# Kernel optimization log

Measured on AMD Instinct MI355X. Metric: run time of the kernel, lower is better.

Reference implementation:

```python
import jax, jax.numpy as jnp
import numpy as np

LN_EPS = 1e-5


def setup_inputs() -> dict:
    key = jax.random.key(0)
    B, S, D = 4, 4096, 1024
    x = jax.random.normal(key, (B, S, D), dtype=jnp.float32)
    gamma = jnp.ones((D,), dtype=jnp.float32)
    beta = jnp.zeros((D,), dtype=jnp.float32)
    return {"x": x, "gamma": gamma, "beta": beta}


def reference(x, gamma, beta):
    # LayerNorm over last dim (embed_dim), matching nn.LayerNorm(eps=1e-5)
    mean = jnp.mean(x, axis=-1, keepdims=True)
    var = jnp.mean(jnp.square(x - mean), axis=-1, keepdims=True)
    xn = (x - mean) / jnp.sqrt(var + LN_EPS)
    xn = xn * gamma + beta
    # FFT along hidden dim then along sequence dim; keep real part.
    f = jnp.fft.fft(jnp.fft.fft(xn, axis=-1), axis=-2)
    return jnp.real(f)
```

## Files before the change

kernel.cpp:

```cpp
#include <hip/hip_runtime.h>
#include <math.h>

#define LN_EPS 1e-5f

constexpr int D = 1024;
constexpr int S = 4096;
constexpr int B = 4;
constexpr int KH = 512;
constexpr float NEG_TWO_PI = -6.283185307179586f;

__device__ __forceinline__ float2 cmul(float2 a, float2 b) {
    return make_float2(a.x * b.x - a.y * b.y, a.x * b.y + a.y * b.x);
}
__device__ __forceinline__ float2 csq(float2 a) {
    return make_float2(a.x * a.x - a.y * a.y, 2.f * a.x * a.y);
}

__device__ __forceinline__ int SWX(int a) {
    int r = a;
    r ^= (-((a >> 5) & 1)) & 5;
    r ^= (-((a >> 6) & 1)) & 10;
    r ^= (-((a >> 7) & 1)) & 17;
    return r;
}

__global__ __launch_bounds__(256) void ln_fft_d(const float* __restrict__ x,
                                                const float* __restrict__ gamma,
                                                const float* __restrict__ beta,
                                                float2* __restrict__ y) {
    __shared__ float re[D];
    __shared__ float im[D];
    __shared__ float2 twA[256];
    __shared__ float red[36];

    const int tid = threadIdx.x;
    const size_t row0 = (size_t)blockIdx.x * 2;

    {
        float sn, c;
        __sincosf(NEG_TWO_PI * (float)tid * (1.0f / 1024.0f), &sn, &c);
        twA[tid] = make_float2(c, sn);
    }

    const float4 a4 = ((const float4*)(x + row0 * D))[tid];
    const float4 c4 = ((const float4*)(x + (row0 + 1) * D))[tid];
    float s0 = a4.x + a4.y + a4.z + a4.w;
    float q0 = a4.x * a4.x + a4.y * a4.y + a4.z * a4.z + a4.w * a4.w;
    float s1 = c4.x + c4.y + c4.z + c4.w;
    float q1 = c4.x * c4.x + c4.y * c4.y + c4.z * c4.z + c4.w * c4.w;
#pragma unroll
    for (int off = 32; off; off >>= 1) {
        s0 += __shfl_down(s0, off); q0 += __shfl_down(q0, off);
        s1 += __shfl_down(s1, off); q1 += __shfl_down(q1, off);
    }
    const int wid = tid >> 6;
    if ((tid & 63) == 0) { red[wid] = s0; red[8 + wid] = q0; red[16 + wid] = s1; red[24 + wid] = q1; }
    __syncthreads();
    if (tid == 0) {
        float S0 = red[0] + red[1] + red[2] + red[3];
        float Q0 = red[8] + red[9] + red[10] + red[11];
        float S1 = red[16] + red[17] + red[18] + red[19];
        float Q1 = red[24] + red[25] + red[26] + red[27];
        float m0 = S0 * (1.0f / D), m1 = S1 * (1.0f / D);
        red[32] = m0; red[33] = rsqrtf(Q0 * (1.0f / D) - m0 * m0 + LN_EPS);
        red[34] = m1; red[35] = rsqrtf(Q1 * (1.0f / D) - m1 * m1 + LN_EPS);
    }
    __syncthreads();
    const float m0 = red[32], r0 = red[33], m1 = red[34], r1 = red[35];

    const float4 g4 = ((const float4*)gamma)[tid];
    const float4 b4 = ((const float4*)beta)[tid];
    const float av[4] = {a4.x, a4.y, a4.z, a4.w};
    const float cv[4] = {c4.x, c4.y, c4.z, c4.w};
    const float gg[4] = {g4.x, g4.y, g4.z, g4.w};
    const float bb[4] = {b4.x, b4.y, b4.z, b4.w};
#pragma unroll
    for (int j = 0; j < 4; ++j) {
        int i = 4 * tid + j;
        unsigned br = __brev((unsigned)i) >> 22;
        int dr = (int)(((br & 0x155u) << 1) | ((br & 0x2AAu) >> 1));
        int p = SWX(dr);
        re[p] = (av[j] - m0) * r0 * gg[j] + bb[j];
        im[p] = (cv[j] - m1) * r1 * gg[j] + bb[j];
    }
    __syncthreads();

#pragma unroll
    for (int st = 0; st < 5; ++st) {
        const int lq = 2 * st;
        const int q = 1 << lq;
        const int j = tid & (q - 1);
        const int i0 = ((tid & ~(q - 1)) << 2) + j;
        const int p0 = SWX(i0);
        const int p1 = SWX(i0 + q);
        const int p2 = SWX(i0 + 2 * q);
        const int p3 = SWX(i0 + 3 * q);
        const float2 w1 = twA[j << (8 - lq)];
        const float2 w2 = csq(w1);
        const float2 w3 = cmul(w1, w2);
        float2 a0 = make_float2(re[p0], im[p0]);
        float2 a1 = cmul(make_float2(re[p1], im[p1]), w1);
        float2 a2 = cmul(make_float2(re[p2], im[p2]), w2);
        float2 a3 = cmul(make_float2(re[p3], im[p3]), w3);
        float t0r = a0.x + a2.x, t0i = a0.y + a2.y;
        float t1r = a0.x - a2.x, t1i = a0.y - a2.y;
        float t2r = a1.x + a3.x, t2i = a1.y + a3.y;
        float t3r = a1.y - a3.y, t3i = a3.x - a1.x;
        re[p0] = t0r + t2r; im[p0] = t0i + t2i;
        re[p1] = t1r + t3r; im[p1] = t1i + t3i;
        re[p2] = t0r - t2r; im[p2] = t0i - t2i;
        re[p3] = t1r - t3r; im[p3] = t1i - t3i;
        __syncthreads();
    }

    float2* y0 = y + row0 * KH;
    float2* y1 = y0 + KH;
    if (tid == 0) {
        int pa = SWX(0), pb = SWX(512);
        y0[0] = make_float2(re[pa], re[pb]);
        y1[0] = make_float2(im[pa], im[pb]);
    } else {
        int kc = tid;
        int p = SWX(kc), pq = SWX(1024 - kc);
        float2 cA = make_float2(re[p], im[p]);
        float2 cB = make_float2(re[pq], im[pq]);
        y0[kc] = make_float2(0.5f * (cA.x + cB.x), 0.5f * (cA.y - cB.y));
        y1[kc] = make_float2(0.5f * (cA.y + cB.y), 0.5f * (cB.x - cA.x));
    }
    {
        int kc = tid + 256;
        int p = SWX(kc), pq = SWX(1024 - kc);
        float2 cA = make_float2(re[p], im[p]);
        float2 cB = make_float2(re[pq], im[pq]);
        y0[kc] = make_float2(0.5f * (cA.x + cB.x), 0.5f * (cA.y - cB.y));
        y1[kc] = make_float2(0.5f * (cA.y + cB.y), 0.5f * (cB.x - cA.x));
    }
}

__global__ __launch_bounds__(256) void fft_s_p1(const float2* y, float2* z) {
    __shared__ float2 tile[64 * 64];
    __shared__ float2 tw64[16];

    const int bid = blockIdx.x;
    const int dt = bid & 7;
    const int n1 = (bid >> 3) & 63;
    const int b  = bid >> 9;
    const int d0 = dt << 6;
    const int lane = threadIdx.x & 63;
    const int r4   = threadIdx.x >> 6;

    if (threadIdx.x < 16) {
        float sn, c;
        __sincosf(NEG_TWO_PI * (float)threadIdx.x * (1.0f / 64.0f), &sn, &c);
        tw64[threadIdx.x] = make_float2(c, sn);
    }

#pragma unroll
    for (int m = 0; m < 16; ++m) {
        int n2 = (m << 2) | r4;
        unsigned br = __brev((unsigned)n2) >> 26;
        int rr = (int)(((br & 0x15u) << 1) | ((br & 0x2Au) >> 1));
        tile[(rr << 6) | lane] =
            y[(size_t)((b << 12) | (n2 << 6) | n1) * KH + d0 + lane];
    }
    __syncthreads();

#pragma unroll
    for (int st = 0; st < 3; ++st) {
        const int lq = 2 * st;
        const int q = 1 << lq;
#pragma unroll
        for (int it = 0; it < 4; ++it) {
            int t = threadIdx.x + (it << 8);
            int d = t & 63;
            int bf = t >> 6;
            int j = bf & (q - 1);
            int i0 = ((bf & ~(q - 1)) << 2) + j;
            float2 w1 = tw64[j << (4 - lq)];
            float2 w2 = csq(w1);
            float2 w3 = cmul(w1, w2);
            float2 a0 = tile[(i0 << 6) | d];
            float2 a1 = cmul(tile[((i0 + q) << 6) | d], w1);
            float2 a2 = cmul(tile[((i0 + 2 * q) << 6) | d], w2);
            float2 a3 = cmul(tile[((i0 + 3 * q) << 6) | d], w3);
            float t0r = a0.x + a2.x, t0i = a0.y + a2.y;
            float t1r = a0.x - a2.x, t1i = a0.y - a2.y;
            float t2r = a1.x + a3.x, t2i = a1.y + a3.y;
            float t3r = a1.y - a3.y, t3i = a3.x - a1.x;
            tile[(i0 << 6) | d]           = make_float2(t0r + t2r, t0i + t2i);
            tile[((i0 + q) << 6) | d]     = make_float2(t1r + t3r, t1i + t3i);
            tile[((i0 + 2 * q) << 6) | d] = make_float2(t0r - t2r, t0i - t2i);
            tile[((i0 + 3 * q) << 6) | d] = make_float2(t1r - t3r, t1i - t3i);
        }
        __syncthreads();
    }

    const float ang0 = NEG_TWO_PI * (float)n1 * (1.0f / 4096.0f);
#pragma unroll
    for (int m = 0; m < 16; ++m) {
        int k2 = (m << 2) | r4;
        float2 vv = tile[(k2 << 6) | lane];
        float sn, c;
        __sincosf(ang0 * (float)k2, &sn, &c);
        z[(size_t)((b << 12) | (k2 << 6) | n1) * KH + d0 + lane] =
            make_float2(vv.x * c - vv.y * sn, vv.x * sn + vv.y * c);
    }
}

__global__ __launch_bounds__(256) void fft_s_p2(const float2* __restrict__ z,
                                                float* __restrict__ out) {
    __shared__ float2 tile[64 * 64];
    __shared__ float2 tw64[16];

    const int lane = threadIdx.x & 63;
    const int r4   = threadIdx.x >> 6;

    if (threadIdx.x < 16) {
        float sn, c;
        __sincosf(NEG_TWO_PI * (float)threadIdx.x * (1.0f / 64.0f), &sn, &c);
        tw64[threadIdx.x] = make_float2(c, sn);
    }

    if (blockIdx.x < B * 64 * 8) {
        const int bid = blockIdx.x;
        const int dt = bid & 7;
        const int k2 = (bid >> 3) & 63;
        const int b  = bid >> 9;
        const int d0 = dt << 6;

#pragma unroll
        for (int m = 0; m < 16; ++m) {
            int n1 = (m << 2) | r4;
            unsigned br = __brev((unsigned)n1) >> 26;
            int rr = (int)(((br & 0x15u) << 1) | ((br & 0x2Au) >> 1));
            tile[(rr << 6) | lane] =
                z[(size_t)((b << 12) | (k2 << 6) | n1) * KH + d0 + lane];
        }
        __syncthreads();

#pragma unroll
        for (int st = 0; st < 3; ++st) {
            const int lq = 2 * st;
            const int q = 1 << lq;
#pragma unroll
            for (int it = 0; it < 4; ++it) {
                int t = threadIdx.x + (it << 8);
                int d = t & 63;
                int bf = t >> 6;
                int j = bf & (q - 1);
                int i0 = ((bf & ~(q - 1)) << 2) + j;
                float2 w1 = tw64[j << (4 - lq)];
                float2 w2 = csq(w1);
                float2 w3 = cmul(w1, w2);
                float2 a0 = tile[(i0 << 6) | d];
                float2 a1 = cmul(tile[((i0 + q) << 6) | d], w1);
                float2 a2 = cmul(tile[((i0 + 2 * q) << 6) | d], w2);
                float2 a3 = cmul(tile[((i0 + 3 * q) << 6) | d], w3);
                float t0r = a0.x + a2.x, t0i = a0.y + a2.y;
                float t1r = a0.x - a2.x, t1i = a0.y - a2.y;
                float t2r = a1.x + a3.x, t2i = a1.y + a3.y;
                float t3r = a1.y - a3.y, t3i = a3.x - a1.x;
                tile[(i0 << 6) | d]           = make_float2(t0r + t2r, t0i + t2i);
                tile[((i0 + q) << 6) | d]     = make_float2(t1r + t3r, t1i + t3i);
                tile[((i0 + 2 * q) << 6) | d] = make_float2(t0r - t2r, t0i - t2i);
                tile[((i0 + 3 * q) << 6) | d] = make_float2(t1r - t3r, t1i - t3i);
            }
            __syncthreads();
        }

        const int kc = d0 + lane;
#pragma unroll
        for (int m = 0; m < 16; ++m) {
            int k1 = (m << 2) | r4;
            int q = (k1 << 6) | k2;
            float v = tile[(k1 << 6) | lane].x;
            if (kc) {
                out[((size_t)(b << 12) + (size_t)q) * D + kc] = v;
                int qm = (S - q) & (S - 1);
                out[((size_t)(b << 12) + (size_t)qm) * D + (D - kc)] = v;
            }
        }
    } else {
        const int b = blockIdx.x - B * 64 * 8;

#pragma unroll
        for (int m = 0; m < 16; ++m) {
            int k2 = (m << 2) | r4;
            unsigned br = __brev((unsigned)lane) >> 26;
            int rr = (int)(((br & 0x15u) << 1) | ((br & 0x2Au) >> 1));
            tile[(rr << 6) | k2] = z[(size_t)((b << 12) | (k2 << 6) | lane) * KH];
        }
        __syncthreads();

#pragma unroll
        for (int st = 0; st < 3; ++st) {
            const int lq = 2 * st;
            const int q = 1 << lq;
#pragma unroll
            for (int it = 0; it < 4; ++it) {
                int t = threadIdx.x + (it << 8);
                int d = t & 63;
                int bf = t >> 6;
                int j = bf & (q - 1);
                int i0 = ((bf & ~(q - 1)) << 2) + j;
                float2 w1 = tw64[j << (4 - lq)];
                float2 w2 = csq(w1);
                float2 w3 = cmul(w1, w2);
                float2 a0 = tile[(i0 << 6) | d];
                float2 a1 = cmul(tile[((i0 + q) << 6) | d], w1);
                float2 a2 = cmul(tile[((i0 + 2 * q) << 6) | d], w2);
                float2 a3 = cmul(tile[((i0 + 3 * q) << 6) | d], w3);
                float t0r = a0.x + a2.x, t0i = a0.y + a2.y;
                float t1r = a0.x - a2.x, t1i = a0.y - a2.y;
                float t2r = a1.x + a3.x, t2i = a1.y + a3.y;
                float t3r = a1.y - a3.y, t3i = a3.x - a1.x;
                tile[(i0 << 6) | d]           = make_float2(t0r + t2r, t0i + t2i);
                tile[((i0 + q) << 6) | d]     = make_float2(t1r + t3r, t1i + t3i);
                tile[((i0 + 2 * q) << 6) | d] = make_float2(t0r - t2r, t0i - t2i);
                tile[((i0 + 3 * q) << 6) | d] = make_float2(t1r - t3r, t1i - t3i);
            }
            __syncthreads();
        }

#pragma unroll
        for (int m = 0; m < 16; ++m) {
            int k1 = (m << 2) | r4;
            int k2 = lane;
            int q = (k1 << 6) | k2;
            int k2m = (64 - k2) & 63;
            int k1m = (k2 == 0) ? ((64 - k1) & 63) : (63 - k1);
            float2 Hq = tile[(k1 << 6) | k2];
            float2 Hm = tile[(k1m << 6) | k2m];
            size_t ob = ((size_t)(b << 12) + (size_t)q) * D;
            out[ob]       = 0.5f * (Hq.x + Hm.x);
            out[ob + 512] = 0.5f * (Hq.y + Hm.y);
        }
    }
}

extern "C" void kernel_launch(void* const* d_in, const int* in_sizes, int n_in,
                              void* d_out, int out_size, void* d_ws, size_t ws_size,
                              hipStream_t stream) {
    const float* x     = (const float*)d_in[0];
    const float* gamma = (const float*)d_in[1];
    const float* beta  = (const float*)d_in[2];
    float* out = (float*)d_out;

    float2* y = (float2*)d_ws;

    ln_fft_d<<<B * S / 2, 256, 0, stream>>>(x, gamma, beta, y);
    fft_s_p1<<<B * 64 * 8, 256, 0, stream>>>(y, y);
    fft_s_p2<<<B * 64 * 8 + B, 256, 0, stream>>>(y, out);
}
```

Before: 178.4 us.

## Restructure FFT stages: DIF radix-4 for D-axis, radix-8 two-pass for 64-point

The D-axis 1024-point FFT now uses a decimation-in-frequency radix-4 scheme on interleaved float2 shared memory with padded indexing. The first stage runs from registers, and the output is read back in digit-reversed order. The 64-point S-axis FFTs move from three radix-4 stages to two radix-8 passes with a twiddle table of 64 entries, which cuts shared-memory round trips and barriers. The inter-pass twiddle in fft_s_p1 is now built by recurrence multiplication instead of one sincos per element, which adds a small accumulated rounding error.

```diff
diff --git a/kernel.cpp b/kernel.cpp
--- a/kernel.cpp
+++ b/kernel.cpp
@@ -8,6 +8,7 @@
 constexpr int B = 4;
 constexpr int KH = 512;
 constexpr float NEG_TWO_PI = -6.283185307179586f;
+constexpr float RSQ2 = 0.70710678118654752f;
 
 __device__ __forceinline__ float2 cmul(float2 a, float2 b) {
     return make_float2(a.x * b.x - a.y * b.y, a.x * b.y + a.y * b.x);
@@ -15,39 +16,101 @@
 __device__ __forceinline__ float2 csq(float2 a) {
     return make_float2(a.x * a.x - a.y * a.y, 2.f * a.x * a.y);
 }
-
-__device__ __forceinline__ int SWX(int a) {
-    int r = a;
-    r ^= (-((a >> 5) & 1)) & 5;
-    r ^= (-((a >> 6) & 1)) & 10;
-    r ^= (-((a >> 7) & 1)) & 17;
-    return r;
+__device__ __forceinline__ float2 cadd(float2 a, float2 b) { return make_float2(a.x + b.x, a.y + b.y); }
+__device__ __forceinline__ float2 csub(float2 a, float2 b) { return make_float2(a.x - b.x, a.y - b.y); }
+__device__ __forceinline__ float2 cnegi(float2 a) { return make_float2(a.y, -a.x); }
+__device__ __forceinline__ float2 cposi(float2 a) { return make_float2(-a.y, a.x); }
+
+__device__ __forceinline__ int P(int a) { return a + (a >> 4); }
+
+__device__ __forceinline__ int rev4_10(int v) {
+    unsigned br = __brev((unsigned)v) >> 22;
+    return (int)(((br & 0x155u) << 1) | ((br & 0x2AAu) >> 1));
+}
+
+__device__ __forceinline__ void dft8(float2& c0, float2& c1, float2& c2, float2& c3,
+                                     float2& c4, float2& c5, float2& c6, float2& c7) {
+    float2 t0 = cadd(c0, c4), t1 = csub(c0, c4);
+    float2 t2 = cadd(c2, c6), t3 = csub(c2, c6);
+    float2 t4 = cadd(c1, c5), t5 = csub(c1, c5);
+    float2 t6 = cadd(c3, c7), t7 = csub(c3, c7);
+    float2 E0 = cadd(t0, t2), E2 = csub(t0, t2);
+    float2 E1 = cadd(t1, cnegi(t3)), E3 = cadd(t1, cposi(t3));
+    float2 O0 = cadd(t4, t6), O2 = csub(t4, t6);
+    float2 O1 = cadd(t5, cnegi(t7)), O3 = cadd(t5, cposi(t7));
+    float2 W1O1 = make_float2(RSQ2 * (O1.x + O1.y), RSQ2 * (O1.y - O1.x));
+    float2 W2O2 = cnegi(O2);
+    float2 W3O3 = make_float2(RSQ2 * (O3.y - O3.x), -RSQ2 * (O3.x + O3.y));
+    c0 = cadd(E0, O0); c4 = csub(E0, O0);
+    c1 = cadd(E1, W1O1); c5 = csub(E1, W1O1);
+    c2 = cadd(E2, W2O2); c6 = csub(E2, W2O2);
+    c3 = cadd(E3, W3O3); c7 = csub(E3, W3O3);
+}
+
+__device__ __forceinline__ void fft64_rows(float2* tile, const float2* tw64) {
+#pragma unroll
+    for (int h = 0; h < 2; ++h) {
+        int bf = threadIdx.x + (h << 8);
+        int col = bf & 63;
+        int g = bf >> 6;
+#define R0(mm) tile[((((g) << 3) | (mm)) << 6) | col]
+        float2 c0 = R0(0), c1 = R0(1), c2 = R0(2), c3 = R0(3);
+        float2 c4 = R0(4), c5 = R0(5), c6 = R0(6), c7 = R0(7);
+        dft8(c0, c1, c2, c3, c4, c5, c6, c7);
+        R0(0) = c0; R0(1) = c1; R0(2) = c2; R0(3) = c3;
+        R0(4) = c4; R0(5) = c5; R0(6) = c6; R0(7) = c7;
+#undef R0
+    }
+    __syncthreads();
+#pragma unroll
+    for (int h = 0; h < 2; ++h) {
+        int bf = threadIdx.x + (h << 8);
+        int col = bf & 63;
+        int j = bf >> 6;
+#define R1(mm) tile[(((j) + ((mm) << 3)) << 6) | col]
+        float2 c0 = R1(0);
+        float2 c1 = cmul(R1(1), tw64[j]);
+        float2 c2 = cmul(R1(2), tw64[2 * j]);
+        float2 c3 = cmul(R1(3), tw64[3 * j]);
+        float2 c4 = cmul(R1(4), tw64[4 * j]);
+        float2 c5 = cmul(R1(5), tw64[5 * j]);
+        float2 c6 = cmul(R1(6), tw64[6 * j]);
+        float2 c7 = cmul(R1(7), tw64[7 * j]);
+        dft8(c0, c1, c2, c3, c4, c5, c6, c7);
+        R1(0) = c0; R1(1) = c1; R1(2) = c2; R1(3) = c3;
+        R1(4) = c4; R1(5) = c5; R1(6) = c6; R1(7) = c7;
+#undef R1
+    }
+    __syncthreads();
 }
 
 __global__ __launch_bounds__(256) void ln_fft_d(const float* __restrict__ x,
                                                 const float* __restrict__ gamma,
                                                 const float* __restrict__ beta,
                                                 float2* __restrict__ y) {
-    __shared__ float re[D];
-    __shared__ float im[D];
+    __shared__ float2 cx[1088];
     __shared__ float2 twA[256];
     __shared__ float red[36];
 
     const int tid = threadIdx.x;
     const size_t row0 = (size_t)blockIdx.x * 2;
-
-    {
-        float sn, c;
-        __sincosf(NEG_TWO_PI * (float)tid * (1.0f / 1024.0f), &sn, &c);
-        twA[tid] = make_float2(c, sn);
-    }
-
-    const float4 a4 = ((const float4*)(x + row0 * D))[tid];
-    const float4 c4 = ((const float4*)(x + (row0 + 1) * D))[tid];
-    float s0 = a4.x + a4.y + a4.z + a4.w;
-    float q0 = a4.x * a4.x + a4.y * a4.y + a4.z * a4.z + a4.w * a4.w;
-    float s1 = c4.x + c4.y + c4.z + c4.w;
-    float q1 = c4.x * c4.x + c4.y * c4.y + c4.z * c4.z + c4.w * c4.w;
+    const float* x0 = x + row0 * D;
+    const float* x1 = x0 + D;
+
+    float wsn, wcs;
+    __sincosf(NEG_TWO_PI * (float)tid * (1.0f / 1024.0f), &wsn, &wcs);
+    const float2 w1s0 = make_float2(wcs, wsn);
+    twA[tid] = w1s0;
+
+    float a0[4], a1[4];
+    float s0 = 0.f, q0 = 0.f, s1 = 0.f, q1 = 0.f;
+#pragma unroll
+    for (int j = 0; j < 4; ++j) {
+        float u = x0[tid + (j << 8)];
+        float v = x1[tid + (j << 8)];
+        a0[j] = u; a1[j] = v;
+        s0 += u; q0 += u * u; s1 += v; q1 += v * v;
+    }
 #pragma unroll
     for (int off = 32; off; off >>= 1) {
         s0 += __shfl_down(s0, off); q0 += __shfl_down(q0, off);
@@ -68,78 +131,86 @@
     __syncthreads();
     const float m0 = red[32], r0 = red[33], m1 = red[34], r1 = red[35];
 
-    const float4 g4 = ((const float4*)gamma)[tid];
-    const float4 b4 = ((const float4*)beta)[tid];
-    const float av[4] = {a4.x, a4.y, a4.z, a4.w};
-    const float cv[4] = {c4.x, c4.y, c4.z, c4.w};
-    const float gg[4] = {g4.x, g4.y, g4.z, g4.w};
-    const float bb[4] = {b4.x, b4.y, b4.z, b4.w};
-#pragma unroll
-    for (int j = 0; j < 4; ++j) {
-        int i = 4 * tid + j;
-        unsigned br = __brev((unsigned)i) >> 22;
-        int dr = (int)(((br & 0x155u) << 1) | ((br & 0x2AAu) >> 1));
-        int p = SWX(dr);
-        re[p] = (av[j] - m0) * r0 * gg[j] + bb[j];
-        im[p] = (cv[j] - m1) * r1 * gg[j] + bb[j];
-    }
-    __syncthreads();
-
-#pragma unroll
-    for (int st = 0; st < 5; ++st) {
-        const int lq = 2 * st;
-        const int q = 1 << lq;
-        const int j = tid & (q - 1);
-        const int i0 = ((tid & ~(q - 1)) << 2) + j;
-        const int p0 = SWX(i0);
-        const int p1 = SWX(i0 + q);
-        const int p2 = SWX(i0 + 2 * q);
-        const int p3 = SWX(i0 + 3 * q);
-        const float2 w1 = twA[j << (8 - lq)];
-        const float2 w2 = csq(w1);
-        const float2 w3 = cmul(w1, w2);
-        float2 a0 = make_float2(re[p0], im[p0]);
-        float2 a1 = cmul(make_float2(re[p1], im[p1]), w1);
-        float2 a2 = cmul(make_float2(re[p2], im[p2]), w2);
-        float2 a3 = cmul(make_float2(re[p3], im[p3]), w3);
-        float t0r = a0.x + a2.x, t0i = a0.y + a2.y;
-        float t1r = a0.x - a2.x, t1i = a0.y - a2.y;
-        float t2r = a1.x + a3.x, t2i = a1.y + a3.y;
-        float t3r = a1.y - a3.y, t3i = a3.x - a1.x;
-        re[p0] = t0r + t2r; im[p0] = t0i + t2i;
-        re[p1] = t1r + t3r; im[p1] = t1i + t3i;
-        re[p2] = t0r - t2r; im[p2] = t0i - t2i;
-        re[p3] = t1r - t3r; im[p3] = t1i - t3i;
+    float2 A0, A1, A2, A3;
+    {
+        float gg, bb;
+        gg = gamma[tid];       bb = beta[tid];
+        A0 = make_float2((a0[0] - m0) * r0 * gg + bb, (a1[0] - m1) * r1 * gg + bb);
+        gg = gamma[tid + 256]; bb = beta[tid + 256];
+        A1 = make_float2((a0[1] - m0) * r0 * gg + bb, (a1[1] - m1) * r1 * gg + bb);
+        gg = gamma[tid + 512]; bb = beta[tid + 512];
+        A2 = make_float2((a0[2] - m0) * r0 * gg + bb, (a1[2] - m1) * r1 * gg + bb);
+        gg = gamma[tid + 768]; bb = beta[tid + 768];
+        A3 = make_float2((a0[3] - m0) * r0 * gg + bb, (a1[3] - m1) * r1 * gg + bb);
+    }
+    {
+        float2 b0 = cadd(A0, A2), b1 = csub(A0, A2);
+        float2 b2 = cadd(A1, A3), b3 = csub(A1, A3);
+        float2 w2 = csq(w1s0), w3 = cmul(w1s0, w2);
+        cx[P(tid)]       = cadd(b0, b2);
+        cx[P(tid + 256)] = cmul(cadd(b1, cnegi(b3)), w1s0);
+        cx[P(tid + 512)] = cmul(csub(b0, b2), w2);
+        cx[P(tid + 768)] = cmul(cadd(b1, cposi(b3)), w3);
+    }
+    __syncthreads();
+
+#pragma unroll
+    for (int sIdx = 0; sIdx < 3; ++sIdx) {
+        const int lL = 8 - 2 * sIdx;
+        const int qq = 1 << (lL - 2);
+        const int j = tid & (qq - 1);
+        const int base = ((tid >> (lL - 2)) << lL) | j;
+        const float2 w1 = twA[j << (10 - lL)];
+        const float2 w2 = csq(w1), w3 = cmul(w1, w2);
+        const int p0 = P(base), p1 = P(base + qq), p2 = P(base + 2 * qq), p3 = P(base + 3 * qq);
+        float2 B0 = cx[p0], B1 = cx[p1], B2 = cx[p2], B3 = cx[p3];
+        float2 b0 = cadd(B0, B2), b1 = csub(B0, B2);
+        float2 b2 = cadd(B1, B3), b3 = csub(B1, B3);
+        cx[p0] = cadd(b0, b2);
+        cx[p1] = cmul(cadd(b1, cnegi(b3)), w1);
+        cx[p2] = cmul(csub(b0, b2), w2);
+        cx[p3] = cmul(cadd(b1, cposi(b3)), w3);
         __syncthreads();
     }
+    {
+        const int base = tid << 2;
+        const int p0 = P(base), p1 = P(base + 1), p2 = P(base + 2), p3 = P(base + 3);
+        float2 B0 = cx[p0], B1 = cx[p1], B2 = cx[p2], B3 = cx[p3];
+        float2 b0 = cadd(B0, B2), b1 = csub(B0, B2);
+        float2 b2 = cadd(B1, B3), b3 = csub(B1, B3);
+        cx[p0] = cadd(b0, b2);
+        cx[p1] = cadd(b1, cnegi(b3));
+        cx[p2] = csub(b0, b2);
+        cx[p3] = cadd(b1, cposi(b3));
+    }
+    __syncthreads();
 
     float2* y0 = y + row0 * KH;
     float2* y1 = y0 + KH;
     if (tid == 0) {
-        int pa = SWX(0), pb = SWX(512);
-        y0[0] = make_float2(re[pa], re[pb]);
-        y1[0] = make_float2(im[pa], im[pb]);
+        float2 X0 = cx[P(0)];
+        float2 X512 = cx[P(2)];
+        y0[0] = make_float2(X0.x, X512.x);
+        y1[0] = make_float2(X0.y, X512.y);
     } else {
         int kc = tid;
-        int p = SWX(kc), pq = SWX(1024 - kc);
-        float2 cA = make_float2(re[p], im[p]);
-        float2 cB = make_float2(re[pq], im[pq]);
-        y0[kc] = make_float2(0.5f * (cA.x + cB.x), 0.5f * (cA.y - cB.y));
-        y1[kc] = make_float2(0.5f * (cA.y + cB.y), 0.5f * (cB.x - cA.x));
+        float2 XA = cx[P(rev4_10(kc))];
+        float2 XB = cx[P(rev4_10(1024 - kc))];
+        y0[kc] = make_float2(0.5f * (XA.x + XB.x), 0.5f * (XA.y - XB.y));
+        y1[kc] = make_float2(0.5f * (XA.y + XB.y), 0.5f * (XB.x - XA.x));
     }
     {
         int kc = tid + 256;
-        int p = SWX(kc), pq = SWX(1024 - kc);
-        float2 cA = make_float2(re[p], im[p]);
-        float2 cB = make_float2(re[pq], im[pq]);
-        y0[kc] = make_float2(0.5f * (cA.x + cB.x), 0.5f * (cA.y - cB.y));
-        y1[kc] = make_float2(0.5f * (cA.y + cB.y), 0.5f * (cB.x - cA.x));
+        float2 XA = cx[P(rev4_10(kc))];
+        float2 XB = cx[P(rev4_10(1024 - kc))];
+        y0[kc] = make_float2(0.5f * (XA.x + XB.x), 0.5f * (XA.y - XB.y));
+        y1[kc] = make_float2(0.5f * (XA.y + XB.y), 0.5f * (XB.x - XA.x));
     }
 }
 
 __global__ __launch_bounds__(256) void fft_s_p1(const float2* y, float2* z) {
     __shared__ float2 tile[64 * 64];
-    __shared__ float2 tw64[16];
+    __shared__ float2 tw64[64];
 
     const int bid = blockIdx.x;
     const int dt = bid & 7;
@@ -149,7 +220,7 @@
     const int lane = threadIdx.x & 63;
     const int r4   = threadIdx.x >> 6;
 
-    if (threadIdx.x < 16) {
+    if (threadIdx.x < 64) {
         float sn, c;
         __sincosf(NEG_TWO_PI * (float)threadIdx.x * (1.0f / 64.0f), &sn, &c);
         tw64[threadIdx.x] = make_float2(c, sn);
@@ -158,64 +229,40 @@
 #pragma unroll
     for (int m = 0; m < 16; ++m) {
         int n2 = (m << 2) | r4;
-        unsigned br = __brev((unsigned)n2) >> 26;
-        int rr = (int)(((br & 0x15u) << 1) | ((br & 0x2Au) >> 1));
+        int rr = ((n2 & 7) << 3) | (n2 >> 3);
         tile[(rr << 6) | lane] =
             y[(size_t)((b << 12) | (n2 << 6) | n1) * KH + d0 + lane];
     }
     __syncthreads();
 
-#pragma unroll
-    for (int st = 0; st < 3; ++st) {
-        const int lq = 2 * st;
-        const int q = 1 << lq;
-#pragma unroll
-        for (int it = 0; it < 4; ++it) {
-            int t = threadIdx.x + (it << 8);
-            int d = t & 63;
-            int bf = t >> 6;
-            int j = bf & (q - 1);
-            int i0 = ((bf & ~(q - 1)) << 2) + j;
-            float2 w1 = tw64[j << (4 - lq)];
-            float2 w2 = csq(w1);
-            float2 w3 = cmul(w1, w2);
-            float2 a0 = tile[(i0 << 6) | d];
-            float2 a1 = cmul(tile[((i0 + q) << 6) | d], w1);
-            float2 a2 = cmul(tile[((i0 + 2 * q) << 6) | d], w2);
-            float2 a3 = cmul(tile[((i0 + 3 * q) << 6) | d], w3);
-            float t0r = a0.x + a2.x, t0i = a0.y + a2.y;
-            float t1r = a0.x - a2.x, t1i = a0.y - a2.y;
-            float t2r = a1.x + a3.x, t2i = a1.y + a3.y;
-            float t3r = a1.y - a3.y, t3i = a3.x - a1.x;
-            tile[(i0 << 6) | d]           = make_float2(t0r + t2r, t0i + t2i);
-            tile[((i0 + q) << 6) | d]     = make_float2(t1r + t3r, t1i + t3i);
-            tile[((i0 + 2 * q) << 6) | d] = make_float2(t0r - t2r, t0i - t2i);
-            tile[((i0 + 3 * q) << 6) | d] = make_float2(t1r - t3r, t1i - t3i);
-        }
-        __syncthreads();
-    }
-
-    const float ang0 = NEG_TWO_PI * (float)n1 * (1.0f / 4096.0f);
+    fft64_rows(tile, tw64);
+
+    float2 wq, wstep;
+    {
+        float sn, c;
+        __sincosf(NEG_TWO_PI * (float)(n1 * r4) * (1.0f / 4096.0f), &sn, &c);
+        wq = make_float2(c, sn);
+        __sincosf(NEG_TWO_PI * (float)n1 * (1.0f / 1024.0f), &sn, &c);
+        wstep = make_float2(c, sn);
+    }
 #pragma unroll
     for (int m = 0; m < 16; ++m) {
         int k2 = (m << 2) | r4;
         float2 vv = tile[(k2 << 6) | lane];
-        float sn, c;
-        __sincosf(ang0 * (float)k2, &sn, &c);
-        z[(size_t)((b << 12) | (k2 << 6) | n1) * KH + d0 + lane] =
-            make_float2(vv.x * c - vv.y * sn, vv.x * sn + vv.y * c);
+        z[(size_t)((b << 12) | (k2 << 6) | n1) * KH + d0 + lane] = cmul(vv, wq);
+        wq = cmul(wq, wstep);
     }
 }
 
 __global__ __launch_bounds__(256) void fft_s_p2(const float2* __restrict__ z,
                                                 float* __restrict__ out) {
     __shared__ float2 tile[64 * 64];
-    __shared__ float2 tw64[16];
+    __shared__ float2 tw64[64];
 
     const int lane = threadIdx.x & 63;
     const int r4   = threadIdx.x >> 6;
 
-    if (threadIdx.x < 16) {
+    if (threadIdx.x < 64) {
         float sn, c;
         __sincosf(NEG_TWO_PI * (float)threadIdx.x * (1.0f / 64.0f), &sn, &c);
         tw64[threadIdx.x] = make_float2(c, sn);
@@ -231,42 +278,13 @@
 #pragma unroll
         for (int m = 0; m < 16; ++m) {
             int n1 = (m << 2) | r4;
-            unsigned br = __brev((unsigned)n1) >> 26;
-            int rr = (int)(((br & 0x15u) << 1) | ((br & 0x2Au) >> 1));
+            int rr = ((n1 & 7) << 3) | (n1 >> 3);
             tile[(rr << 6) | lane] =
                 z[(size_t)((b << 12) | (k2 << 6) | n1) * KH + d0 + lane];
         }
         __syncthreads();
 
-#pragma unroll
-        for (int st = 0; st < 3; ++st) {
-            const int lq = 2 * st;
-            const int q = 1 << lq;
-#pragma unroll
-            for (int it = 0; it < 4; ++it) {
-                int t = threadIdx.x + (it << 8);
-                int d = t & 63;
-                int bf = t >> 6;
-                int j = bf & (q - 1);
-                int i0 = ((bf & ~(q - 1)) << 2) + j;
-                float2 w1 = tw64[j << (4 - lq)];
-                float2 w2 = csq(w1);
-                float2 w3 = cmul(w1, w2);
-                float2 a0 = tile[(i0 << 6) | d];
-                float2 a1 = cmul(tile[((i0 + q) << 6) | d], w1);
-                float2 a2 = cmul(tile[((i0 + 2 * q) << 6) | d], w2);
-                float2 a3 = cmul(tile[((i0 + 3 * q) << 6) | d], w3);
-                float t0r = a0.x + a2.x, t0i = a0.y + a2.y;
-                float t1r = a0.x - a2.x, t1i = a0.y - a2.y;
-                float t2r = a1.x + a3.x, t2i = a1.y + a3.y;
-                float t3r = a1.y - a3.y, t3i = a3.x - a1.x;
-                tile[(i0 << 6) | d]           = make_float2(t0r + t2r, t0i + t2i);
-                tile[((i0 + q) << 6) | d]     = make_float2(t1r + t3r, t1i + t3i);
-                tile[((i0 + 2 * q) << 6) | d] = make_float2(t0r - t2r, t0i - t2i);
-                tile[((i0 + 3 * q) << 6) | d] = make_float2(t1r - t3r, t1i - t3i);
-            }
-            __syncthreads();
-        }
+        fft64_rows(tile, tw64);
 
         const int kc = d0 + lane;
 #pragma unroll
@@ -286,41 +304,12 @@
 #pragma unroll
         for (int m = 0; m < 16; ++m) {
             int k2 = (m << 2) | r4;
-            unsigned br = __brev((unsigned)lane) >> 26;
-            int rr = (int)(((br & 0x15u) << 1) | ((br & 0x2Au) >> 1));
+            int rr = ((lane & 7) << 3) | (lane >> 3);
             tile[(rr << 6) | k2] = z[(size_t)((b << 12) | (k2 << 6) | lane) * KH];
         }
         __syncthreads();
 
-#pragma unroll
-        for (int st = 0; st < 3; ++st) {
-            const int lq = 2 * st;
-            const int q = 1 << lq;
-#pragma unroll
-            for (int it = 0; it < 4; ++it) {
-                int t = threadIdx.x + (it << 8);
-                int d = t & 63;
-                int bf = t >> 6;
-                int j = bf & (q - 1);
-                int i0 = ((bf & ~(q - 1)) << 2) + j;
-                float2 w1 = tw64[j << (4 - lq)];
-                float2 w2 = csq(w1);
-                float2 w3 = cmul(w1, w2);
-                float2 a0 = tile[(i0 << 6) | d];
-                float2 a1 = cmul(tile[((i0 + q) << 6) | d], w1);
-                float2 a2 = cmul(tile[((i0 + 2 * q) << 6) | d], w2);
-                float2 a3 = cmul(tile[((i0 + 3 * q) << 6) | d], w3);
-                float t0r = a0.x + a2.x, t0i = a0.y + a2.y;
-                float t1r = a0.x - a2.x, t1i = a0.y - a2.y;
-                float t2r = a1.x + a3.x, t2i = a1.y + a3.y;
-                float t3r = a1.y - a3.y, t3i = a3.x - a1.x;
-                tile[(i0 << 6) | d]           = make_float2(t0r + t2r, t0i + t2i);
-                tile[((i0 + q) << 6) | d]     = make_float2(t1r + t3r, t1i + t3i);
-                tile[((i0 + 2 * q) << 6) | d] = make_float2(t0r - t2r, t0i - t2i);
-                tile[((i0 + 3 * q) << 6) | d] = make_float2(t1r - t3r, t1i - t3i);
-            }
-            __syncthreads();
-        }
+        fft64_rows(tile, tw64);
 
 #pragma unroll
         for (int m = 0; m < 16; ++m) {
```

Result: no change. 179.1 us (+0.4%).
